# Performance work log

Measured on AMD Instinct MI355X. Metric: run time of the kernel, lower is better.

## Reference

```python
import jax, jax.numpy as jnp
import numpy as np

B, N, M, H = 16, 2048, 512, 512


def setup_inputs() -> dict:
    key = jax.random.key(0)
    ks = jax.random.split(key, 14)
    s = 0.02  # weight init scale
    return {
        "A": jax.random.uniform(ks[0], (B, N, N), dtype=jnp.float32),
        "h": jax.random.normal(ks[1], (B, N, M), dtype=jnp.float32),
        # fcv: Linear(m,H) -> ReLU -> Linear(H,H); weights stored [in,out]
        "Wv1": jax.random.normal(ks[2], (M, H), dtype=jnp.float32) * s,
        "bv1": jnp.zeros((H,), jnp.float32),
        "Wv2": jax.random.normal(ks[3], (H, H), dtype=jnp.float32) * s,
        "bv2": jnp.zeros((H,), jnp.float32),
        "Wk": jax.random.normal(ks[4], (M, H), dtype=jnp.float32) * s,
        "bk": jnp.zeros((H,), jnp.float32),
        "Wq": jax.random.normal(ks[5], (M, H), dtype=jnp.float32) * s,
        "bq": jnp.zeros((H,), jnp.float32),
        "Wout": jax.random.normal(ks[6], (H, M), dtype=jnp.float32) * s,
        "bout": jnp.zeros((M,), jnp.float32),
    }


def reference(A, h, Wv1, bv1, Wv2, bv2, Wk, bk, Wq, bq, Wout, bout):
    # v = relu(fcv(h)) where fcv = Lin -> ReLU -> Lin
    v = jax.nn.relu(jax.nn.relu(h @ Wv1 + bv1) @ Wv2 + bv2)      # [B,N,H]
    q = jax.nn.relu(h @ Wq + bq)                                  # [B,N,H]
    k = jax.nn.relu(h @ Wk + bk)                                  # [B,N,H]
    # att = softmax((q @ k^T) * -A, axis=2)
    scores = jnp.einsum("bnh,bmh->bnm", q, k) * -A                # [B,N,N]
    att = jax.nn.softmax(scores, axis=2)
    out = jnp.einsum("bnm,bmh->bnh", att, v) + v                  # [B,N,H]
    return jax.nn.relu(out @ Wout + bout)                         # [B,N,M]
```

## Files before the change

### kernel.cpp

```cpp
#include <hip/hip_runtime.h>

typedef __bf16 bf16;
typedef bf16 bf16x4 __attribute__((ext_vector_type(4)));
typedef bf16 bf16x8 __attribute__((ext_vector_type(8)));
typedef float f32x4 __attribute__((ext_vector_type(4)));

static constexpr int BATCH = 16;
static constexpr int SEQ   = 2048;
static constexpr int DH    = 512;
static constexpr int ROWS  = BATCH * SEQ;

__device__ __forceinline__ f32x4 mfma16(bf16x8 a, bf16x8 b, f32x4 c) {
    return __builtin_amdgcn_mfma_f32_16x16x32_bf16(a, b, c, 0, 0, 0);
}

__device__ __forceinline__ void gl_lds16(const void* g, void* l) {
    __builtin_amdgcn_global_load_lds((const __attribute__((address_space(1))) void*)g,
                                     (__attribute__((address_space(3))) void*)l, 16, 0, 0);
}

__global__ void cvt_all_kernel(const float* __restrict__ h,
                               const float* __restrict__ w0, const float* __restrict__ w1,
                               const float* __restrict__ w2, const float* __restrict__ w3,
                               const float* __restrict__ w4,
                               bf16* __restrict__ hb, bf16* __restrict__ wout) {
    const int b = blockIdx.x;
    if (b < 4096) {
        const int n4 = ROWS * 512 / 4;
        int i = b * 256 + threadIdx.x;
        const int stride = 4096 * 256;
        for (; i < n4; i += stride) {
            f32x4 f = *reinterpret_cast<const f32x4*>(h + (size_t)i * 4);
            bf16x4 o;
            o[0] = (bf16)f[0]; o[1] = (bf16)f[1]; o[2] = (bf16)f[2]; o[3] = (bf16)f[3];
            *reinterpret_cast<bf16x4*>(hb + (size_t)i * 4) = o;
        }
    } else {
        const int bb = b - 4096;
        const int t = bb >> 10;
        const float* in = (t == 0) ? w0 : (t == 1) ? w1 : (t == 2) ? w2 : (t == 3) ? w3 : w4;
        int idx = (bb & 1023) * 256 + threadIdx.x;
        int n = idx >> 9, k = idx & 511;
        wout[t * 262144 + idx] = (bf16)in[k * 512 + n];
    }
}

template <int OMODE>
__global__ __launch_bounds__(256, 2)
void gemm_relu_kernel(const bf16* __restrict__ X, const bf16* __restrict__ Wt,
                      const float* __restrict__ bias,
                      bf16* __restrict__ Y, bf16* __restrict__ Yt,
                      float* __restrict__ Yf)
{
    __shared__ bf16 Xl[2][128 * 64];
    __shared__ bf16 Wl[2][128 * 64];

    const int tid = threadIdx.x;
    const int lane = tid & 63, wid = tid >> 6;
    const int wr = wid >> 1, wc = wid & 1;
    const int id = blockIdx.x;
    const int r0 = (((id >> 5) << 3) + (id & 7)) * 128;
    const int c0 = ((id >> 3) & 3) * 128;
    const int lrow = lane & 15, lhi = lane >> 4;

    const int srow = tid >> 3;
    const int skb  = (tid & 7) ^ (srow & 7);
    const int sdst = wid * 512;

    auto stage = [&](int buf, int kc) {
        const bf16* xs = X + (size_t)r0 * 512 + kc * 64;
        const bf16* ws = Wt + (size_t)c0 * 512 + kc * 64;
        #pragma unroll
        for (int c = 0; c < 4; ++c) {
            const int row = c * 32 + srow;
            gl_lds16(xs + (size_t)row * 512 + skb * 8, &Xl[buf][c * 2048 + sdst]);
        }
        #pragma unroll
        for (int c = 0; c < 4; ++c) {
            const int row = c * 32 + srow;
            gl_lds16(ws + (size_t)row * 512 + skb * 8, &Wl[buf][c * 2048 + sdst]);
        }
    };

    f32x4 acc[4][4] = {};

    stage(0, 0);

    for (int t = 0; t < 8; ++t) {
        const int buf = t & 1;
        if (t + 1 < 8) {
            stage(buf ^ 1, t + 1);
            asm volatile("s_waitcnt vmcnt(8)" ::: "memory");
        } else {
            asm volatile("s_waitcnt vmcnt(0)" ::: "memory");
        }
        __builtin_amdgcn_s_barrier();
        __builtin_amdgcn_sched_barrier(0);

        #pragma unroll
        for (int kk = 0; kk < 2; ++kk) {
            bf16x8 af[4], bfr[4];
            const int kb = kk * 4 + lhi;
            #pragma unroll
            for (int tt = 0; tt < 4; ++tt) {
                const int ra = wr * 64 + tt * 16 + lrow;
                af[tt] = *reinterpret_cast<const bf16x8*>(&Xl[buf][ra * 64 + ((kb ^ (ra & 7)) * 8)]);
            }
            #pragma unroll
            for (int tt = 0; tt < 4; ++tt) {
                const int rb = wc * 64 + tt * 16 + lrow;
                bfr[tt] = *reinterpret_cast<const bf16x8*>(&Wl[buf][rb * 64 + ((kb ^ (rb & 7)) * 8)]);
            }
            #pragma unroll
            for (int i = 0; i < 4; ++i)
                #pragma unroll
                for (int j = 0; j < 4; ++j)
                    acc[i][j] = mfma16(af[i], bfr[j], acc[i][j]);
        }

        asm volatile("s_waitcnt lgkmcnt(0)" ::: "memory");
        __builtin_amdgcn_s_barrier();
        __builtin_amdgcn_sched_barrier(0);
    }

    #pragma unroll
    for (int i = 0; i < 4; ++i) {
        #pragma unroll
        for (int j = 0; j < 4; ++j) {
            const int col = c0 + wc * 64 + j * 16 + lrow;
            const float bb = bias[col];
            #pragma unroll
            for (int rg = 0; rg < 4; ++rg) {
                const int r = r0 + wr * 64 + i * 16 + lhi * 4 + rg;
                float y = acc[i][j][rg] + bb;
                y = y > 0.f ? y : 0.f;
                if (OMODE == 2) {
                    Yf[(size_t)r * 512 + col] = y;
                } else {
                    Y[(size_t)r * 512 + col] = (bf16)y;
                    if (OMODE == 1) {
                        const int bi = r >> 11, nn = r & 2047;
                        Yt[((size_t)bi * 512 + col) * 2048 + nn] = (bf16)y;
                    }
                }
            }
        }
    }
}

__global__ __launch_bounds__(512, 1)
void attn_kernel(const bf16* __restrict__ Q, const bf16* __restrict__ K,
                 const bf16* __restrict__ Vt, const bf16* __restrict__ V,
                 const float* __restrict__ A, bf16* __restrict__ O)
{
    __shared__ bf16 K_lds[128 * 512];
    __shared__ bf16 P_lds[64 * 128];
    __shared__ float sump_lds[2][64];

    const int tid = threadIdx.x;
    const int lane = tid & 63, wid = tid >> 6;
    const int wr = wid >> 1, wc = wid & 1;
    const int lrow = lane & 15, lhi = lane >> 4;

    const int id = blockIdx.x;
    const int xcd = id & 7, j = id >> 3;
    const int bb = 2 * xcd + (j >> 5);
    const int n0 = (j & 31) * 64;
    const int srow_base = wr * 16 + lhi * 4;

    const bf16* Kbase  = K + (size_t)bb * SEQ * DH;
    const bf16* Vtbase = Vt + (size_t)bb * DH * SEQ;

    #pragma unroll
    for (int c = 0; c < 16; ++c) {
        const int row = wid * 16 + c;
        gl_lds16(Kbase + (size_t)row * DH + ((lane ^ (row & 7)) * 8), &K_lds[row * 512]);
    }

    bf16x8 qf[16];
    {
        const bf16* qp = Q + (size_t)(bb * SEQ + n0 + wr * 16 + lrow) * DH + lhi * 8;
        #pragma unroll
        for (int kk = 0; kk < 16; ++kk)
            qf[kk] = *reinterpret_cast<const bf16x8*>(qp + kk * 32);
    }

    float l_part[4] = {};
    f32x4 acc[4][4] = {};

    __syncthreads();

    for (int it = 0; it < 16; ++it) {
        const int m0 = it * 128;

        float av[16];
        {
            const float* ap = A + ((size_t)bb * SEQ + n0 + srow_base) * SEQ + m0 + wc * 64 + lrow;
            #pragma unroll
            for (int sc = 0; sc < 4; ++sc)
                #pragma unroll
                for (int rg = 0; rg < 4; ++rg)
                    av[sc * 4 + rg] = ap[(size_t)rg * SEQ + sc * 16];
        }

        f32x4 s[4] = {};
        {
            __builtin_amdgcn_s_setprio(1);
            #pragma unroll
            for (int kk = 0; kk < 16; ++kk) {
                const int ks = kk * 4 + lhi;
                #pragma unroll
                for (int sc = 0; sc < 4; ++sc) {
                    const int kr = wc * 64 + sc * 16 + lrow;
                    bf16x8 kf = *reinterpret_cast<const bf16x8*>(
                        &K_lds[kr * 512 + ((ks ^ (kr & 7)) * 8)]);
                    s[sc] = mfma16(qf[kk], kf, s[sc]);
                }
            }
            __builtin_amdgcn_s_setprio(0);
        }

        #pragma unroll
        for (int sc = 0; sc < 4; ++sc) {
            #pragma unroll
            for (int rg = 0; rg < 4; ++rg) {
                const float p = __expf(s[sc][rg] * (-av[sc * 4 + rg]));
                const int row = srow_base + rg;
                const int blk = wc * 8 + sc * 2 + (lrow >> 3);
                P_lds[row * 128 + ((blk ^ (row & 7)) * 8) + (lrow & 7)] = (bf16)p;
                l_part[rg] += p;
            }
        }

        asm volatile("s_waitcnt lgkmcnt(0)" ::: "memory");
        __builtin_amdgcn_s_barrier();
        __builtin_amdgcn_sched_barrier(0);

        if (it + 1 < 16) {
            #pragma unroll
            for (int c = 0; c < 16; ++c) {
                const int row = wid * 16 + c;
                gl_lds16(Kbase + (size_t)(m0 + 128 + row) * DH + ((lane ^ (row & 7)) * 8),
                         &K_lds[row * 512]);
            }
        }

        {
            const bf16* vp = Vtbase + (size_t)(wid * 64 + lrow) * SEQ + m0 + lhi * 8;
            bf16x8 vfk[2][4];
            #pragma unroll
            for (int ht = 0; ht < 4; ++ht)
                vfk[0][ht] = *reinterpret_cast<const bf16x8*>(vp + (size_t)(ht * 16) * SEQ);
            #pragma unroll
            for (int kc = 0; kc < 4; ++kc) {
                if (kc + 1 < 4) {
                    #pragma unroll
                    for (int ht = 0; ht < 4; ++ht)
                        vfk[(kc + 1) & 1][ht] = *reinterpret_cast<const bf16x8*>(
                            vp + (size_t)(ht * 16) * SEQ + (kc + 1) * 32);
                }
                __builtin_amdgcn_s_setprio(1);
                #pragma unroll
                for (int t = 0; t < 4; ++t) {
                    const int prow = t * 16 + lrow;
                    const bf16x8 pf = *reinterpret_cast<const bf16x8*>(
                        &P_lds[prow * 128 + (((kc * 4 + lhi) ^ (prow & 7)) * 8)]);
                    #pragma unroll
                    for (int ht = 0; ht < 4; ++ht)
                        acc[t][ht] = mfma16(pf, vfk[kc & 1][ht], acc[t][ht]);
                }
                __builtin_amdgcn_s_setprio(0);
            }
        }

        asm volatile("s_waitcnt lgkmcnt(0)" ::: "memory");
        __builtin_amdgcn_s_barrier();
        __builtin_amdgcn_sched_barrier(0);
    }

    #pragma unroll
    for (int rg = 0; rg < 4; ++rg) {
        float sv = l_part[rg];
        sv += __shfl_xor(sv, 1);
        sv += __shfl_xor(sv, 2);
        sv += __shfl_xor(sv, 4);
        sv += __shfl_xor(sv, 8);
        if (lrow == 0) sump_lds[wc][srow_base + rg] = sv;
    }
    __syncthreads();

    #pragma unroll
    for (int t = 0; t < 4; ++t) {
        #pragma unroll
        for (int rg = 0; rg < 4; ++rg) {
            const int row = t * 16 + lhi * 4 + rg;
            const float inv = 1.f / (sump_lds[0][row] + sump_lds[1][row]);
            const size_t rbase = (size_t)(bb * SEQ + n0 + row) * DH;
            #pragma unroll
            for (int ht = 0; ht < 4; ++ht) {
                const int col = wid * 64 + ht * 16 + lrow;
                const float vv = (float)V[rbase + col];
                O[rbase + col] = (bf16)(acc[t][ht][rg] * inv + vv);
            }
        }
    }
}

extern "C" void kernel_launch(void* const* d_in, const int* in_sizes, int n_in,
                              void* d_out, int out_size, void* d_ws, size_t ws_size,
                              hipStream_t stream) {
    const float* A    = (const float*)d_in[0];
    const float* h    = (const float*)d_in[1];
    const float* Wv1  = (const float*)d_in[2];
    const float* bv1  = (const float*)d_in[3];
    const float* Wv2  = (const float*)d_in[4];
    const float* bv2  = (const float*)d_in[5];
    const float* Wk   = (const float*)d_in[6];
    const float* bk   = (const float*)d_in[7];
    const float* Wq   = (const float*)d_in[8];
    const float* bq   = (const float*)d_in[9];
    const float* Wout = (const float*)d_in[10];
    const float* bout = (const float*)d_in[11];
    float* out = (float*)d_out;

    char* ws = (char*)d_ws;
    const size_t SZ = (size_t)ROWS * 512 * sizeof(bf16);
    bf16* hb   = (bf16*)(ws + 0 * SZ);
    bf16* tq   = (bf16*)(ws + 1 * SZ);
    bf16* kb   = (bf16*)(ws + 2 * SZ);
    bf16* vb   = (bf16*)(ws + 3 * SZ);
    bf16* vtb  = (bf16*)(ws + 4 * SZ);
    bf16* wbase = (bf16*)(ws + 5 * SZ);
    bf16* Wv1t  = wbase + 0 * 262144;
    bf16* Wv2t  = wbase + 1 * 262144;
    bf16* Wqt   = wbase + 2 * 262144;
    bf16* Wkt   = wbase + 3 * 262144;
    bf16* Woutt = wbase + 4 * 262144;
    bf16* ob = hb;

    cvt_all_kernel<<<9216, 256, 0, stream>>>(h, Wv1, Wv2, Wq, Wk, Wout, hb, wbase);

    gemm_relu_kernel<0><<<1024, 256, 0, stream>>>(hb, Wv1t, bv1, tq, nullptr, nullptr);
    gemm_relu_kernel<1><<<1024, 256, 0, stream>>>(tq, Wv2t, bv2, vb, vtb, nullptr);
    gemm_relu_kernel<0><<<1024, 256, 0, stream>>>(hb, Wqt, bq, tq, nullptr, nullptr);
    gemm_relu_kernel<0><<<1024, 256, 0, stream>>>(hb, Wkt, bk, kb, nullptr, nullptr);

    attn_kernel<<<dim3(512), 512, 0, stream>>>(tq, kb, vtb, vb, A, ob);

    gemm_relu_kernel<2><<<1024, 256, 0, stream>>>(ob, Woutt, bout, nullptr, nullptr, out);
}
```

Before: 450.1 us.

## Fuse three h-projection GEMMs into one kernel and stage V-transpose stores through LDS

The three GEMMs that read h (Wv1, Wq, Wk) now run in one kernel where each block loops over the three weight matrices, keeping its X row tile hot in L2 and dropping two launches. The transposed V write in the second fcv GEMM, which was a scattered 2-byte store per element, is now staged in padded shared memory and written out as 16-byte coalesced rows. Workspace buffers are remapped so vt reuses hb and the attention output reuses tb. The fused kernel runs its three GEMMs serially per block, so there is less overlap between them, and it adds an extra barrier plus LDS traffic for the transpose.

```diff
diff --git a/kernel.cpp b/kernel.cpp
--- a/kernel.cpp
+++ b/kernel.cpp
@@ -45,6 +45,111 @@
     }
 }
 
+__global__ __launch_bounds__(256, 2)
+void gemm_tqk_kernel(const bf16* __restrict__ X,
+                     const bf16* __restrict__ Wt0, const bf16* __restrict__ Wt1,
+                     const bf16* __restrict__ Wt2,
+                     const float* __restrict__ b0, const float* __restrict__ b1,
+                     const float* __restrict__ b2,
+                     bf16* __restrict__ Y0, bf16* __restrict__ Y1, bf16* __restrict__ Y2)
+{
+    __shared__ bf16 smem[32768];
+
+    const int tid = threadIdx.x;
+    const int lane = tid & 63, wid = tid >> 6;
+    const int wr = wid >> 1, wc = wid & 1;
+    const int id = blockIdx.x;
+    const int r0 = (((id >> 5) << 3) + (id & 7)) * 128;
+    const int c0 = ((id >> 3) & 3) * 128;
+    const int lrow = lane & 15, lhi = lane >> 4;
+
+    const int srow = tid >> 3;
+    const int skb  = (tid & 7) ^ (srow & 7);
+    const int sdst = wid * 512;
+
+    for (int w = 0; w < 3; ++w) {
+        const bf16* Wt = (w == 0) ? Wt0 : (w == 1) ? Wt1 : Wt2;
+        const float* bias = (w == 0) ? b0 : (w == 1) ? b1 : b2;
+        bf16* Y = (w == 0) ? Y0 : (w == 1) ? Y1 : Y2;
+
+        auto stage = [&](int buf, int kc) {
+            const bf16* xs = X + (size_t)r0 * 512 + kc * 64;
+            const bf16* ws = Wt + (size_t)c0 * 512 + kc * 64;
+            bf16* Xl = smem + buf * 8192;
+            bf16* Wl = smem + 16384 + buf * 8192;
+            #pragma unroll
+            for (int c = 0; c < 4; ++c) {
+                const int row = c * 32 + srow;
+                gl_lds16(xs + (size_t)row * 512 + skb * 8, Xl + c * 2048 + sdst);
+            }
+            #pragma unroll
+            for (int c = 0; c < 4; ++c) {
+                const int row = c * 32 + srow;
+                gl_lds16(ws + (size_t)row * 512 + skb * 8, Wl + c * 2048 + sdst);
+            }
+        };
+
+        f32x4 acc[4][4] = {};
+
+        stage(0, 0);
+
+        for (int t = 0; t < 8; ++t) {
+            const int buf = t & 1;
+            if (t + 1 < 8) {
+                stage(buf ^ 1, t + 1);
+                asm volatile("s_waitcnt vmcnt(8)" ::: "memory");
+            } else {
+                asm volatile("s_waitcnt vmcnt(0)" ::: "memory");
+            }
+            __builtin_amdgcn_s_barrier();
+            __builtin_amdgcn_sched_barrier(0);
+
+            const bf16* Xl = smem + buf * 8192;
+            const bf16* Wl = smem + 16384 + buf * 8192;
+            #pragma unroll
+            for (int kk = 0; kk < 2; ++kk) {
+                bf16x8 af[4], bfr[4];
+                const int kb = kk * 4 + lhi;
+                #pragma unroll
+                for (int tt = 0; tt < 4; ++tt) {
+                    const int ra = wr * 64 + tt * 16 + lrow;
+                    af[tt] = *reinterpret_cast<const bf16x8*>(&Xl[ra * 64 + ((kb ^ (ra & 7)) * 8)]);
+                }
+                #pragma unroll
+                for (int tt = 0; tt < 4; ++tt) {
+                    const int rb = wc * 64 + tt * 16 + lrow;
+                    bfr[tt] = *reinterpret_cast<const bf16x8*>(&Wl[rb * 64 + ((kb ^ (rb & 7)) * 8)]);
+                }
+                #pragma unroll
+                for (int i = 0; i < 4; ++i)
+                    #pragma unroll
+                    for (int j = 0; j < 4; ++j)
+                        acc[i][j] = mfma16(af[i], bfr[j], acc[i][j]);
+            }
+
+            asm volatile("s_waitcnt lgkmcnt(0)" ::: "memory");
+            __builtin_amdgcn_s_barrier();
+            __builtin_amdgcn_sched_barrier(0);
+        }
+
+        #pragma unroll
+        for (int i = 0; i < 4; ++i) {
+            #pragma unroll
+            for (int j = 0; j < 4; ++j) {
+                const int col = c0 + wc * 64 + j * 16 + lrow;
+                const float bb = bias[col];
+                #pragma unroll
+                for (int rg = 0; rg < 4; ++rg) {
+                    const int r = r0 + wr * 64 + i * 16 + lhi * 4 + rg;
+                    float y = acc[i][j][rg] + bb;
+                    y = y > 0.f ? y : 0.f;
+                    Y[(size_t)r * 512 + col] = (bf16)y;
+                }
+            }
+        }
+    }
+}
+
 template <int OMODE>
 __global__ __launch_bounds__(256, 2)
 void gemm_relu_kernel(const bf16* __restrict__ X, const bf16* __restrict__ Wt,
@@ -52,8 +157,7 @@
                       bf16* __restrict__ Y, bf16* __restrict__ Yt,
                       float* __restrict__ Yf)
 {
-    __shared__ bf16 Xl[2][128 * 64];
-    __shared__ bf16 Wl[2][128 * 64];
+    __shared__ bf16 smem[32768];
 
     const int tid = threadIdx.x;
     const int lane = tid & 63, wid = tid >> 6;
@@ -70,15 +174,17 @@
     auto stage = [&](int buf, int kc) {
         const bf16* xs = X + (size_t)r0 * 512 + kc * 64;
         const bf16* ws = Wt + (size_t)c0 * 512 + kc * 64;
+        bf16* Xl = smem + buf * 8192;
+        bf16* Wl = smem + 16384 + buf * 8192;
         #pragma unroll
         for (int c = 0; c < 4; ++c) {
             const int row = c * 32 + srow;
-            gl_lds16(xs + (size_t)row * 512 + skb * 8, &Xl[buf][c * 2048 + sdst]);
+            gl_lds16(xs + (size_t)row * 512 + skb * 8, Xl + c * 2048 + sdst);
         }
         #pragma unroll
         for (int c = 0; c < 4; ++c) {
             const int row = c * 32 + srow;
-            gl_lds16(ws + (size_t)row * 512 + skb * 8, &Wl[buf][c * 2048 + sdst]);
+            gl_lds16(ws + (size_t)row * 512 + skb * 8, Wl + c * 2048 + sdst);
         }
     };
 
@@ -97,6 +203,8 @@
         __builtin_amdgcn_s_barrier();
         __builtin_amdgcn_sched_barrier(0);
 
+        const bf16* Xl = smem + buf * 8192;
+        const bf16* Wl = smem + 16384 + buf * 8192;
         #pragma unroll
         for (int kk = 0; kk < 2; ++kk) {
             bf16x8 af[4], bfr[4];
@@ -104,12 +212,12 @@
             #pragma unroll
             for (int tt = 0; tt < 4; ++tt) {
                 const int ra = wr * 64 + tt * 16 + lrow;
-                af[tt] = *reinterpret_cast<const bf16x8*>(&Xl[buf][ra * 64 + ((kb ^ (ra & 7)) * 8)]);
+                af[tt] = *reinterpret_cast<const bf16x8*>(&Xl[ra * 64 + ((kb ^ (ra & 7)) * 8)]);
             }
             #pragma unroll
             for (int tt = 0; tt < 4; ++tt) {
                 const int rb = wc * 64 + tt * 16 + lrow;
-                bfr[tt] = *reinterpret_cast<const bf16x8*>(&Wl[buf][rb * 64 + ((kb ^ (rb & 7)) * 8)]);
+                bfr[tt] = *reinterpret_cast<const bf16x8*>(&Wl[rb * 64 + ((kb ^ (rb & 7)) * 8)]);
             }
             #pragma unroll
             for (int i = 0; i < 4; ++i)
@@ -139,11 +247,23 @@
                 } else {
                     Y[(size_t)r * 512 + col] = (bf16)y;
                     if (OMODE == 1) {
-                        const int bi = r >> 11, nn = r & 2047;
-                        Yt[((size_t)bi * 512 + col) * 2048 + nn] = (bf16)y;
+                        smem[(wc * 64 + j * 16 + lrow) * 136
+                             + (wr * 64 + i * 16 + lhi * 4 + rg)] = (bf16)y;
                     }
                 }
             }
+        }
+    }
+
+    if (OMODE == 1) {
+        __syncthreads();
+        const int hr = tid >> 1, half = tid & 1;
+        const size_t obase = ((size_t)(r0 >> 11) * 512 + c0 + hr) * 2048
+                             + (r0 & 2047) + half * 64;
+        #pragma unroll
+        for (int c = 0; c < 8; ++c) {
+            bf16x8 v = *reinterpret_cast<const bf16x8*>(&smem[hr * 136 + half * 64 + c * 8]);
+            *reinterpret_cast<bf16x8*>(&Yt[obase + c * 8]) = v;
         }
     }
 }
@@ -326,26 +446,27 @@
     char* ws = (char*)d_ws;
     const size_t SZ = (size_t)ROWS * 512 * sizeof(bf16);
     bf16* hb   = (bf16*)(ws + 0 * SZ);
-    bf16* tq   = (bf16*)(ws + 1 * SZ);
-    bf16* kb   = (bf16*)(ws + 2 * SZ);
-    bf16* vb   = (bf16*)(ws + 3 * SZ);
-    bf16* vtb  = (bf16*)(ws + 4 * SZ);
+    bf16* tb   = (bf16*)(ws + 1 * SZ);
+    bf16* qb   = (bf16*)(ws + 2 * SZ);
+    bf16* kb   = (bf16*)(ws + 3 * SZ);
+    bf16* vb   = (bf16*)(ws + 4 * SZ);
     bf16* wbase = (bf16*)(ws + 5 * SZ);
     bf16* Wv1t  = wbase + 0 * 262144;
     bf16* Wv2t  = wbase + 1 * 262144;
     bf16* Wqt   = wbase + 2 * 262144;
     bf16* Wkt   = wbase + 3 * 262144;
     bf16* Woutt = wbase + 4 * 262144;
-    bf16* ob = hb;
+    bf16* vtb = hb;
+    bf16* ob  = tb;
 
     cvt_all_kernel<<<9216, 256, 0, stream>>>(h, Wv1, Wv2, Wq, Wk, Wout, hb, wbase);
 
-    gemm_relu_kernel<0><<<1024, 256, 0, stream>>>(hb, Wv1t, bv1, tq, nullptr, nullptr);
-    gemm_relu_kernel<1><<<1024, 256, 0, stream>>>(tq, Wv2t, bv2, vb, vtb, nullptr);
-    gemm_relu_kernel<0><<<1024, 256, 0, stream>>>(hb, Wqt, bq, tq, nullptr, nullptr);
-    gemm_relu_kernel<0><<<1024, 256, 0, stream>>>(hb, Wkt, bk, kb, nullptr, nullptr);
-
-    attn_kernel<<<dim3(512), 512, 0, stream>>>(tq, kb, vtb, vb, A, ob);
+    gemm_tqk_kernel<<<1024, 256, 0, stream>>>(hb, Wv1t, Wqt, Wkt, bv1, bq, bk,
+                                              tb, qb, kb);
+
+    gemm_relu_kernel<1><<<1024, 256, 0, stream>>>(tb, Wv2t, bv2, vb, vtb, nullptr);
+
+    attn_kernel<<<dim3(512), 512, 0, stream>>>(qb, kb, vtb, vb, A, ob);
 
     gemm_relu_kernel<2><<<1024, 256, 0, stream>>>(ob, Woutt, bout, nullptr, nullptr, out);
 }
```

New measurement: 411.9 us, median of 2. 1.09x faster.
